# Performance work log

Hardware: AMD Instinct MI355X
Metric: run time of the kernel (lower is better)

## Reference

```python
import jax, jax.numpy as jnp
import numpy as np

B, L = 4, 8192
IN_CH, OUT_CH = 1, 1
H = 64               # d_model
NSTATE = 16          # d_state
DBLK = 4             # number of residual blocks
DCONV = 16
EXPAND = 2
DINNER = EXPAND * H              # 128
HEADDIM = H // 4                 # 16
NHEADS = DINNER // HEADDIM       # 8
CONV_DIM = DINNER + 2 * NSTATE   # 160 (ngroups=1)
D_IN_PROJ = 2 * DINNER + 2 * NSTATE + NHEADS  # 296
CHUNK = 128


def setup_inputs():
    key = jax.random.key(0)
    ks = jax.random.split(key, 12)
    rn = lambda k, shape, s: (jax.random.normal(k, shape) * s).astype(jnp.float32)
    x = rn(ks[0], (B, L, IN_CH), 1.0)
    w_in = rn(ks[1], (H, IN_CH), 1.0)
    w_out = rn(ks[2], (OUT_CH, H), 1.0 / np.sqrt(H))
    in_proj_w = rn(ks[3], (DBLK, D_IN_PROJ, H), 1.0 / np.sqrt(H))
    conv_w = rn(ks[4], (DBLK, CONV_DIM, DCONV), 1.0 / np.sqrt(DCONV))
    conv_b = rn(ks[5], (DBLK, CONV_DIM), 0.02)
    dt = jnp.exp(jax.random.uniform(ks[6], (DBLK, NHEADS)) * (np.log(0.1) - np.log(1e-3)) + np.log(1e-3))
    dt_bias = (dt + jnp.log(-jnp.expm1(-dt))).astype(jnp.float32)  # inverse softplus
    A_log = jnp.log(jax.random.uniform(ks[7], (DBLK, NHEADS), minval=1.0, maxval=16.0)).astype(jnp.float32)
    D_skip = jnp.ones((DBLK, NHEADS), jnp.float32)
    init_states = rn(ks[8], (DBLK, NHEADS, HEADDIM, NSTATE), 0.01)
    norm_w = jnp.ones((DBLK, DINNER), jnp.float32)
    out_proj_w = rn(ks[9], (DBLK, H, DINNER), 1.0 / np.sqrt(DINNER))
    mlp_w = rn(ks[10], (DBLK, H, H), 1.0 / np.sqrt(H))
    mlp_b = jnp.zeros((DBLK, H), jnp.float32)
    return {"x": x, "w_in": w_in, "w_out": w_out, "in_proj_w": in_proj_w,
            "conv_w": conv_w, "conv_b": conv_b, "dt_bias": dt_bias, "A_log": A_log,
            "D_skip": D_skip, "init_states": init_states, "norm_w": norm_w,
            "out_proj_w": out_proj_w, "mlp_w": mlp_w, "mlp_b": mlp_b}


def segsum(a):
    # a: (..., q) -> (..., q, q); seg[i, j] = sum_{k=j+1..i} a[k] on lower triangle (diag=0), exp->0 above
    q = a.shape[-1]
    cs = jnp.cumsum(a, axis=-1)
    seg = cs[..., :, None] - cs[..., None, :]
    mask = jnp.tril(jnp.ones((q, q), dtype=bool))
    return jnp.where(mask, seg, -1e30)


def ssd(X, dA, Bm, Cm, init_state):
    # Chunked SSD (Mamba2 paper). X: (b,l,h,p) = x*dt, dA: (b,l,h), Bm/Cm: (b,l,n), init_state: (b,h,p,n)
    b, l, h, p = X.shape
    c = l // CHUNK
    X = X.reshape(b, c, CHUNK, h, p)
    Bm = Bm.reshape(b, c, CHUNK, NSTATE)
    Cm = Cm.reshape(b, c, CHUNK, NSTATE)
    A = dA.reshape(b, c, CHUNK, h).transpose(0, 3, 1, 2)  # (b,h,c,q)
    A_cs = jnp.cumsum(A, axis=-1)
    # intra-chunk (diagonal blocks)
    Lm = jnp.exp(segsum(A))  # (b,h,c,q,q)
    Y_diag = jnp.einsum('bcln,bcsn,bhcls,bcshp->bclhp', Cm, Bm, Lm, X)
    # per-chunk final states
    decay_states = jnp.exp(A_cs[..., -1:] - A_cs)  # (b,h,c,q)
    states = jnp.einsum('bcln,bhcl,bclhp->bchpn', Bm, decay_states, X)
    states = jnp.concatenate([init_state[:, None], states], axis=1)  # (b,c+1,h,p,n)
    # inter-chunk recurrence (vectorized via segsum over chunk decays)
    decay_chunk = jnp.exp(segsum(jnp.pad(A_cs[..., -1], ((0, 0), (0, 0), (1, 0)))))  # (b,h,c+1,c+1)
    new_states = jnp.einsum('bhzc,bchpn->bzhpn', decay_chunk, states)
    prev_states = new_states[:, :-1]  # state entering each chunk
    state_decay = jnp.exp(A_cs)
    Y_off = jnp.einsum('bcln,bchpn,bhcl->bclhp', Cm, prev_states, state_decay)
    return (Y_diag + Y_off).reshape(b, l, h, p)


def mamba2(u, w_inp, cw, cb, dtb, alog, dskip, istate, nw, w_outp):
    b, l, _ = u.shape
    zxbcdt = jnp.einsum('bld,ed->ble', u, w_inp)  # (b,l,296)
    z = zxbcdt[..., :DINNER]
    xBC = zxbcdt[..., DINNER:DINNER + CONV_DIM]
    dt = jax.nn.softplus(zxbcdt[..., DINNER + CONV_DIM:] + dtb)  # (b,l,h)
    # causal depthwise conv over seq + silu
    xBC = jax.lax.conv_general_dilated(
        xBC.transpose(0, 2, 1), cw[:, None, :], (1,), [(DCONV - 1, 0)],
        feature_group_count=CONV_DIM, dimension_numbers=('NCH', 'OIH', 'NCH'))
    xBC = jax.nn.silu(xBC + cb[None, :, None]).transpose(0, 2, 1)
    xs = xBC[..., :DINNER]
    Bm = xBC[..., DINNER:DINNER + NSTATE]
    Cm = xBC[..., DINNER + NSTATE:]
    A = -jnp.exp(alog)  # (h,)
    xh = xs.reshape(b, l, NHEADS, HEADDIM)
    init = jnp.broadcast_to(istate, (b,) + istate.shape)
    y = ssd(xh * dt[..., None], dt * A, Bm, Cm, init)
    y = y + xh * dskip[None, None, :, None]  # D skip
    y = y.reshape(b, l, DINNER)
    # gated RMSNorm: norm(y * silu(z)) * weight
    y = y * jax.nn.silu(z)
    y = y * jax.lax.rsqrt(jnp.mean(y * y, axis=-1, keepdims=True) + 1e-5) * nw
    return jnp.einsum('ble,de->bld', y, w_outp)


def reference(x, w_in, w_out, in_proj_w, conv_w, conv_b, dt_bias, A_log,
              D_skip, init_states, norm_w, out_proj_w, mlp_w, mlp_b):
    h = jnp.einsum('bli,hi->blh', x, w_in)
    for i in range(DBLK):
        y = mamba2(h, in_proj_w[i], conv_w[i], conv_b[i], dt_bias[i], A_log[i],
                   D_skip[i], init_states[i], norm_w[i], out_proj_w[i])
        t = y / jnp.sqrt(1.0 + y * y)  # TanhApprox
        y = jnp.einsum('blh,oh->blo', t, mlp_w[i]) + mlp_b[i]
        h = h + y  # residual
    return jnp.einsum('blh,oh->blo', h, w_out)
```

## Files before the change

### kernel.cpp

```cpp
#include <hip/hip_runtime.h>
#include <math.h>

#define NB 4
#define SEQ 8192
#define NT (NB*SEQ)
#define HDIM 64
#define NST 16
#define NBLK 4
#define KCONV 16
#define DIN 128
#define PDIM 16
#define NH 8
#define CDIM 160
#define EPROJ 296
#define CH 128
#define NC 64

typedef __attribute__((ext_vector_type(8))) short short8;
typedef __attribute__((ext_vector_type(4))) float f32x4;

__device__ __forceinline__ float sigf(float x){ return 1.0f/(1.0f+__expf(-x)); }

__device__ __forceinline__ unsigned short bf16r(float f){
  unsigned int u = __float_as_uint(f);
  u = (u + 0x7fffu + ((u >> 16) & 1u)) >> 16;
  return (unsigned short)u;
}
__device__ __forceinline__ unsigned int pk_bf16(float a, float b){
  return (unsigned int)bf16r(a) | ((unsigned int)bf16r(b) << 16);
}
__device__ __forceinline__ float bf16f(unsigned short h){
  return __uint_as_float(((unsigned int)h) << 16);
}

__global__ __launch_bounds__(256) void k_init(const float* __restrict__ x, const float* __restrict__ w_in,
                                              float* __restrict__ h,
                                              const float* __restrict__ w,
                                              unsigned short* __restrict__ whi,
                                              unsigned short* __restrict__ wlo){
  int bi = blockIdx.x;
  const int HB = (NT*HDIM)/256;
  if(bi < HB){
    int i = bi*256 + threadIdx.x;
    int t = i >> 6, d = i & 63;
    h[i] = x[t]*w_in[d];
  } else {
    int i = (bi - HB)*256 + threadIdx.x;
    if(i < NBLK*EPROJ*HDIM){
      float f = w[i];
      unsigned short hi = bf16r(f);
      float fh = bf16f(hi);
      whi[i] = hi;
      wlo[i] = bf16r(f - fh);
    }
  }
}

__global__ __launch_bounds__(1024) void k_front(const float* __restrict__ h,
                                                const unsigned short* __restrict__ whi,
                                                const unsigned short* __restrict__ wlo,
                                                const float* __restrict__ cw, const float* __restrict__ cb,
                                                const float* __restrict__ dtb, const float* __restrict__ alog,
                                                unsigned short* __restrict__ zxz,
                                                unsigned short* __restrict__ xbc,
                                                float* __restrict__ dt, float* __restrict__ acs,
                                                float* __restrict__ asum, float* __restrict__ S){
  __shared__ __align__(16) unsigned char smf[148480];
  unsigned short* Hh  = (unsigned short*)(smf);
  unsigned short* Hl  = (unsigned short*)(smf + 20736);
  float* zxcS         = (float*)(smf + 41472);
  unsigned short* XhT = (unsigned short*)(smf);
  unsigned short* XlT = (unsigned short*)(smf + 34816);
  unsigned short* BhT = (unsigned short*)(smf + 69632);
  unsigned short* BlT = (unsigned short*)(smf + 73984);
  float* dtraw = (float*)(smf + 136192);
  float* dtl   = (float*)(smf + 140288);
  float* wle   = (float*)(smf + 144384);

  int bc = blockIdx.x;
  int c = bc & 63, b = bc >> 6;
  int t0 = b*SEQ + c*CH;
  int tid = threadIdx.x, lane = tid & 63, wid = tid >> 6;
  int quad = lane >> 4, lq = lane & 15;

#pragma unroll
  for(int k=0;k<3;k++){
    int idx = tid + k*1024;
    if(idx < 2304){
      int tok = idx >> 4;
      int d0 = (idx & 15) * 4;
      float4 v;
      if(c == 0 && tok < 16){ v = make_float4(0.f,0.f,0.f,0.f); }
      else v = *(const float4*)(h + (size_t)(t0 - 16 + tok)*HDIM + d0);
      float vv[4] = {v.x, v.y, v.z, v.w};
      unsigned short hi4[4], lo4[4];
#pragma unroll
      for(int j=0;j<4;j++){
        unsigned short hi = bf16r(vv[j]);
        hi4[j] = hi;
        lo4[j] = bf16r(vv[j] - bf16f(hi));
      }
      uint2 ph, pl;
      ph.x = (unsigned int)hi4[0] | ((unsigned int)hi4[1] << 16);
      ph.y = (unsigned int)hi4[2] | ((unsigned int)hi4[3] << 16);
      pl.x = (unsigned int)lo4[0] | ((unsigned int)lo4[1] << 16);
      pl.y = (unsigned int)lo4[2] | ((unsigned int)lo4[3] << 16);
      *(uint2*)&Hh[tok*72 + d0] = ph;
      *(uint2*)&Hl[tok*72 + d0] = pl;
    }
  }
  __syncthreads();

  {
    int L = wid;
    int tg, et;
    if(L < 152){ tg = 1 + L/19; et = L % 19; } else { tg = 0; et = 8 + (L - 152); }
    {
      int e_a = et*16 + lq;
      int ec = (e_a < EPROJ) ? e_a : (EPROJ-1);
      const unsigned short* wh = whi + (size_t)ec*HDIM + quad*8;
      const unsigned short* wl = wlo + (size_t)ec*HDIM + quad*8;
      short8 ah0 = *(const short8*)wh;
      short8 ah1 = *(const short8*)(wh + 32);
      short8 al0 = *(const short8*)wl;
      short8 al1 = *(const short8*)(wl + 32);
      while(true){
        int Ln = L + 16;
        int tgn = 0, etn = 0;
        short8 nh0 = ah0, nh1 = ah1, nl0 = al0, nl1 = al1;
        if(Ln < 162){
          if(Ln < 152){ tgn = 1 + Ln/19; etn = Ln % 19; } else { tgn = 0; etn = 8 + (Ln - 152); }
          int e_n = etn*16 + lq;
          int ecn = (e_n < EPROJ) ? e_n : (EPROJ-1);
          const unsigned short* wh2 = whi + (size_t)ecn*HDIM + quad*8;
          const unsigned short* wl2 = wlo + (size_t)ecn*HDIM + quad*8;
          nh0 = *(const short8*)wh2;
          nh1 = *(const short8*)(wh2 + 32);
          nl0 = *(const short8*)wl2;
          nl1 = *(const short8*)(wl2 + 32);
        }
        const unsigned short* hrh = Hh + (tg*16 + lq)*72 + quad*8;
        const unsigned short* hrl = Hl + (tg*16 + lq)*72 + quad*8;
        short8 xh0 = *(const short8*)hrh;
        short8 xh1 = *(const short8*)(hrh + 32);
        short8 xl0 = *(const short8*)hrl;
        short8 xl1 = *(const short8*)(hrl + 32);
        f32x4 acc = {0.f,0.f,0.f,0.f};
        acc = __builtin_amdgcn_mfma_f32_16x16x32_bf16(ah0, xh0, acc, 0, 0, 0);
        acc = __builtin_amdgcn_mfma_f32_16x16x32_bf16(ah1, xh1, acc, 0, 0, 0);
        acc = __builtin_amdgcn_mfma_f32_16x16x32_bf16(ah0, xl0, acc, 0, 0, 0);
        acc = __builtin_amdgcn_mfma_f32_16x16x32_bf16(ah1, xl1, acc, 0, 0, 0);
        acc = __builtin_amdgcn_mfma_f32_16x16x32_bf16(al0, xh0, acc, 0, 0, 0);
        acc = __builtin_amdgcn_mfma_f32_16x16x32_bf16(al1, xh1, acc, 0, 0, 0);
        if(tg >= 1){
          int tokg = t0 + (tg-1)*16 + lq;
#pragma unroll
          for(int r=0;r<4;r++){
            int e = et*16 + quad*4 + r;
            if(e < 128)        zxz[(size_t)e*NT + tokg] = bf16r(acc[r]);
            else if(e < 288)   zxcS[(e-128)*148 + tg*16 + lq] = acc[r];
            else if(e < 296)   dtraw[(e-288)*128 + (tg-1)*16 + lq] = acc[r];
          }
        } else {
#pragma unroll
          for(int r=0;r<4;r++){
            int e = et*16 + quad*4 + r;
            zxcS[(e-128)*148 + lq] = acc[r];
          }
        }
        if(Ln >= 162) break;
        L = Ln; tg = tgn; et = etn;
        ah0 = nh0; ah1 = nh1; al0 = nl0; al1 = nl1;
      }
    }
  }
  __syncthreads();

  unsigned int hiP[3][4], loP[3][4];
#pragma unroll
  for(int it=0; it<3; it++){
    int G = tid + it*1024;
    if(G < 2560){
      int ch = G >> 4, sg = (G & 15)*8;
      float buf[24];
#pragma unroll
      for(int q4=0;q4<6;q4++){
        float4 f = *(const float4*)&zxcS[ch*148 + sg + q4*4];
        buf[q4*4+0]=f.x; buf[q4*4+1]=f.y; buf[q4*4+2]=f.z; buf[q4*4+3]=f.w;
      }
      float wv[16];
#pragma unroll
      for(int k=0;k<16;k++) wv[k] = cw[ch*KCONV + k];
      float bias = cb[ch];
      unsigned short hs[8], ls[8];
#pragma unroll
      for(int s=0;s<8;s++){
        float acc = bias;
#pragma unroll
        for(int k=0;k<16;k++) acc += wv[k]*buf[s+1+k];
        float r = acc * sigf(acc);
        unsigned short hi = bf16r(r);
        hs[s] = hi;
        ls[s] = bf16r(r - bf16f(hi));
      }
      hiP[it][0] = (unsigned int)hs[0] | ((unsigned int)hs[1] << 16);
      hiP[it][1] = (unsigned int)hs[2] | ((unsigned int)hs[3] << 16);
      hiP[it][2] = (unsigned int)hs[4] | ((unsigned int)hs[5] << 16);
      hiP[it][3] = (unsigned int)hs[6] | ((unsigned int)hs[7] << 16);
      loP[it][0] = (unsigned int)ls[0] | ((unsigned int)ls[1] << 16);
      loP[it][1] = (unsigned int)ls[2] | ((unsigned int)ls[3] << 16);
      loP[it][2] = (unsigned int)ls[4] | ((unsigned int)ls[5] << 16);
      loP[it][3] = (unsigned int)ls[6] | ((unsigned int)ls[7] << 16);
      uint4 pk;
      pk.x = hiP[it][0]; pk.y = hiP[it][1]; pk.z = hiP[it][2]; pk.w = hiP[it][3];
      *(uint4*)(xbc + (size_t)ch*NT + t0 + sg) = pk;
    }
  }
  {
    int hh = tid >> 7, s = tid & 127;
    float raw = dtraw[hh*128 + s] + dtb[hh];
    float v = (raw > 20.f) ? raw : log1pf(__expf(raw));
    dtl[hh*128 + s] = v;
    dt[(size_t)hh*NT + t0 + s] = v;
  }
  __syncthreads();

#pragma unroll
  for(int it=0; it<3; it++){
    int G = tid + it*1024;
    if(G < 2560){
      int ch = G >> 4, sg = (G & 15)*8;
      if(ch < 128){
        uint4 vh; vh.x=hiP[it][0]; vh.y=hiP[it][1]; vh.z=hiP[it][2]; vh.w=hiP[it][3];
        uint4 vl; vl.x=loP[it][0]; vl.y=loP[it][1]; vl.z=loP[it][2]; vl.w=loP[it][3];
        *(uint4*)&XhT[ch*136 + sg] = vh;
        *(uint4*)&XlT[ch*136 + sg] = vl;
      } else if(ch < 144){
        uint4 vh; vh.x=hiP[it][0]; vh.y=hiP[it][1]; vh.z=hiP[it][2]; vh.w=hiP[it][3];
        uint4 vl; vl.x=loP[it][0]; vl.y=loP[it][1]; vl.z=loP[it][2]; vl.w=loP[it][3];
        *(uint4*)&BhT[(ch-128)*136 + sg] = vh;
        *(uint4*)&BlT[(ch-128)*136 + sg] = vl;
      }
    }
  }
  if(wid < 8){
    int hh = wid;
    float A = -__expf(alog[hh]);
    float2 dd = *(const float2*)&dtl[hh*128 + 2*lane];
    float d0 = dd.x, d1 = dd.y;
    float v0 = d0*A, v1 = d1*A;
    float s = v0 + v1;
    for(int off=1; off<64; off<<=1){
      float o = __shfl_up(s, off);
      if(lane >= off) s += o;
    }
    float tot = __shfl(s, 63);
    float excl = s - (v0+v1);
    float a0 = excl+v0, a1 = excl+v0+v1;
    *(float2*)&acs[(size_t)hh*NT + t0 + 2*lane] = make_float2(a0, a1);
    if(lane == 63) asum[(size_t)bc*NH + hh] = __expf(tot);
    wle[hh*128 + 2*lane]   = d0*__expf(tot - a0);
    wle[hh*128 + 2*lane+1] = d1*__expf(tot - a1);
  }
  __syncthreads();

  if(wid < 8){
    int hh = wid;
    f32x4 acc = {0.f,0.f,0.f,0.f};
#pragma unroll
    for(int kb=0;kb<4;kb++){
      int k0 = kb*32 + quad*8;
      short8 xh = *(const short8*)&XhT[(hh*16 + lq)*136 + k0];
      short8 xl = *(const short8*)&XlT[(hh*16 + lq)*136 + k0];
      float4 w0 = *(const float4*)&wle[hh*128 + k0];
      float4 w1 = *(const float4*)&wle[hh*128 + k0 + 4];
      float wv8[8] = {w0.x,w0.y,w0.z,w0.w,w1.x,w1.y,w1.z,w1.w};
      short8 ah, al;
#pragma unroll
      for(int j=0;j<8;j++){
        float xv = bf16f((unsigned short)xh[j]) + bf16f((unsigned short)xl[j]);
        float pw = xv * wv8[j];
        unsigned short hi = bf16r(pw);
        ah[j] = (short)hi;
        al[j] = (short)bf16r(pw - bf16f(hi));
      }
      short8 bh = *(const short8*)&BhT[lq*136 + k0];
      short8 bl = *(const short8*)&BlT[lq*136 + k0];
      acc = __builtin_amdgcn_mfma_f32_16x16x32_bf16(ah, bh, acc, 0, 0, 0);
      acc = __builtin_amdgcn_mfma_f32_16x16x32_bf16(ah, bl, acc, 0, 0, 0);
      acc = __builtin_amdgcn_mfma_f32_16x16x32_bf16(al, bh, acc, 0, 0, 0);
    }
    float* Sp = S + ((size_t)bc*NH + hh)*256;
#pragma unroll
    for(int r=0;r<4;r++) Sp[(quad*4 + r)*16 + lq] = acc[r];
  }
}

__global__ __launch_bounds__(64) void k_scan(const float* __restrict__ S, const float* __restrict__ easum,
                                             const float* __restrict__ init, float* __restrict__ prev){
  int q  = blockIdx.x & 3;
  int hh = (blockIdx.x >> 2) & 7;
  int b  = blockIdx.x >> 5;
  int el = q*64 + threadIdx.x;
  const size_t cs = (size_t)NH*256;
  const float* Sp = S + ((size_t)(b*NC)*NH + hh)*256 + el;
  float* Pp = prev + ((size_t)(b*NC)*NH + hh)*256 + el;
  const float* ap = easum + (size_t)(b*NC)*NH + hh;
  float e[NC];
#pragma unroll
  for(int c=0;c<NC;c++) e[c] = ap[(size_t)c*NH];
  float r = init[hh*256 + el];
  float s0 = Sp[0], s1 = Sp[cs], s2 = Sp[2*cs], s3 = Sp[3*cs];
#pragma unroll
  for(int c=0;c<NC;c+=4){
    Pp[(size_t)c*cs] = r;
    r = e[c]*r + s0;
    s0 = (c+4 < NC) ? Sp[(size_t)(c+4)*cs] : 0.f;
    Pp[(size_t)(c+1)*cs] = r;
    r = e[c+1]*r + s1;
    s1 = (c+5 < NC) ? Sp[(size_t)(c+5)*cs] : 0.f;
    Pp[(size_t)(c+2)*cs] = r;
    r = e[c+2]*r + s2;
    s2 = (c+6 < NC) ? Sp[(size_t)(c+6)*cs] : 0.f;
    Pp[(size_t)(c+3)*cs] = r;
    r = e[c+3]*r + s3;
    s3 = (c+7 < NC) ? Sp[(size_t)(c+7)*cs] : 0.f;
  }
}

__global__ __launch_bounds__(1024) void k_tail(const unsigned short* __restrict__ xbc,
                                               const unsigned short* __restrict__ zxz,
                                               const float* __restrict__ dt, const float* __restrict__ acs,
                                               const float* __restrict__ prev, const float* __restrict__ dskip,
                                               const float* __restrict__ nw, const float* __restrict__ opw,
                                               const float* __restrict__ mw, const float* __restrict__ mb,
                                               float* __restrict__ h,
                                               int last, const float* __restrict__ wout,
                                               float* __restrict__ out){
  __shared__ __align__(16) unsigned char sm[151840];
  unsigned short* Bb   = (unsigned short*)(sm);
  unsigned short* Cb   = (unsigned short*)(sm + 6144);
  unsigned short* XbT  = (unsigned short*)(sm + 12288);
  unsigned short* P0   = (unsigned short*)(sm + 55296);
  unsigned short* P1   = (unsigned short*)(sm + 98304);
  float* Al  = (float*)(sm + 141312);
  float* Dtl = (float*)(sm + 145408);
  float* nwl = (float*)(sm + 149504);
  float* mbl = (float*)(sm + 150016);
  unsigned short* zbuf = (unsigned short*)(sm + 150272);
  float* ssl  = (float*)(sm + 150304);
  float* outb = (float*)(sm + 151328);
  unsigned short* Zb = XbT;
  unsigned short* Wo = P0;
  unsigned short* Wm = P0 + 64*136;
  unsigned short* Yn = P1;
  unsigned short* Tt = XbT;

  int bc = blockIdx.x;
  int c = bc & 63, b = bc >> 6;
  int t0 = b*SEQ + c*CH;
  int tid = threadIdx.x, lane = tid & 63, wid = tid >> 6;
  int quad = lane >> 4, lq = lane & 15;
  int hgrp = wid >> 3;
  int wr7 = wid & 7;
  int widr = (wr7 < 4) ? wr7 : (11 - wr7);
  int strip = widr*16;

  {
    int ch = tid >> 5;
    int s4 = (tid & 31) * 4;
    uint2 xu = *(const uint2*)&xbc[(size_t)(DIN+ch)*NT + t0 + s4];
    unsigned short v0 = (unsigned short)(xu.x & 0xffffu);
    unsigned short v1 = (unsigned short)(xu.x >> 16);
    unsigned short v2 = (unsigned short)(xu.y & 0xffffu);
    unsigned short v3 = (unsigned short)(xu.y >> 16);
    unsigned short* dst = (ch < 16) ? Bb : Cb;
    int cc = (ch < 16) ? ch : (ch - 16);
    dst[(s4+0)*24 + cc] = v0;
    dst[(s4+1)*24 + cc] = v1;
    dst[(s4+2)*24 + cc] = v2;
    dst[(s4+3)*24 + cc] = v3;
  }
#pragma unroll
  for(int k=0;k<4;k++){
    int fi = tid + k*1024;
    int p = fi >> 5, s4 = fi & 31;
    uint2 xu = *(const uint2*)&xbc[(size_t)p*NT + t0 + s4*4];
    float4 dv = *(const float4*)&dt[(size_t)(p>>4)*NT + t0 + s4*4];
    float x0 = bf16f((unsigned short)(xu.x & 0xffffu));
    float x1 = bf16f((unsigned short)(xu.x >> 16));
    float x2 = bf16f((unsigned short)(xu.y & 0xffffu));
    float x3 = bf16f((unsigned short)(xu.y >> 16));
    *(unsigned int*)&XbT[p*168 + s4*4]   = pk_bf16(x0*dv.x, x1*dv.y);
    *(unsigned int*)&XbT[p*168 + s4*4+2] = pk_bf16(x2*dv.z, x3*dv.w);
  }
#pragma unroll
  for(int k=0;k<2;k++){
    int idx = tid + k*1024;
    int hh = idx >> 8, rest = idx & 255;
    int p = rest >> 4, n = rest & 15;
    XbT[(hh*16+p)*168 + 128 + n] = bf16r(prev[((size_t)bc*NH + hh)*256 + rest]);
  }
#pragma unroll
  for(int k=0;k<2;k++){
    int idx = tid + k*1024;
    if(idx < 1536){
      int p = idx / 12, cc = idx - p*12;
      *(unsigned int*)&XbT[p*168 + 144 + 2*cc] = 0u;
    }
  }
  {
    int hh = tid >> 7, s = tid & 127;
    Al[hh*128+s]  = acs[(size_t)hh*NT + t0 + s];
    Dtl[hh*128+s] = dt[(size_t)hh*NT + t0 + s];
  }
  if(tid < 128) nwl[tid] = nw[tid];
  else if(tid < 192) mbl[tid-128] = mb[tid-128];
  else if(tid < 208) zbuf[tid-192] = 0;
  {
    unsigned short* Pgz = hgrp ? P1 : P0;
#pragma unroll
    for(int k=0;k<3;k++){
      int idx = lane + k*64;
      int rr = idx / 12, cc = idx - rr*12;
      *(unsigned int*)&Pgz[(strip+rr)*168 + 144 + 2*cc] = 0u;
    }
    int zc0 = (widr+1)*16;
    int nu  = (7 - widr)*8;
    for(int u = lane>>4; u < nu; u += 4){
      *(unsigned int*)&Pgz[(strip+(lane&15))*168 + zc0 + 2*u] = 0u;
    }
  }
  __syncthreads();

  short8 afr;
  {
    int row = strip + lq;
    const unsigned short* ap = (quad < 2) ? &Cb[row*24 + quad*8] : zbuf;
    afr = *(const short8*)ap;
  }
  f32x4 sc[8];
#pragma unroll
  for(int nt=0;nt<8;nt++){
    f32x4 acc = {0.f,0.f,0.f,0.f};
    if(nt <= widr){
      const unsigned short* bp = (quad < 2) ? &Bb[(nt*16+lq)*24 + quad*8] : zbuf;
      short8 bfr = *(const short8*)bp;
      acc = __builtin_amdgcn_mfma_f32_16x16x32_bf16(afr, bfr, acc, 0, 0, 0);
    }
    sc[nt] = acc;
  }

  unsigned short* Pg = hgrp ? P1 : P0;
  f32x4 accv[4];
  for(int j=0;j<4;j++){
    int hh2 = hgrp*4 + j;
    const float* Alh = Al + hh2*128;
    float alr[4];
#pragma unroll
    for(int r=0;r<4;r++) alr[r] = Alh[strip + quad*4 + r];
#pragma unroll
    for(int nt=0;nt<8;nt++){
      if(nt <= widr){
        int col = nt*16 + lq;
        float alc = Alh[col];
#pragma unroll
        for(int r=0;r<4;r++){
          int row = strip + quad*4 + r;
          float p = sc[nt][r] * __expf(alr[r] - alc);
          p = (col <= row) ? p : 0.f;
          Pg[row*168 + col] = bf16r(p);
        }
      }
    }
    {
      int n = lane & 15, rg = lane >> 4;
#pragma unroll
      for(int rr=0;rr<4;rr++){
        int row = strip + rg*4 + rr;
        float ea = __expf(Alh[row]);
        Pg[row*168 + 128 + n] = bf16r(bf16f(Cb[row*24+n]) * ea);
      }
    }
    f32x4 acc2 = {0.f,0.f,0.f,0.f};
#pragma unroll
    for(int ks=0;ks<5;ks++){
      short8 bfr = *(const short8*)&XbT[(hh2*16+lq)*168 + ks*32 + quad*8];
      short8 af  = *(const short8*)&Pg[(strip+lq)*168 + ks*32 + quad*8];
      acc2 = __builtin_amdgcn_mfma_f32_16x16x32_bf16(af, bfr, acc2, 0, 0, 0);
    }
    const float* Dth = Dtl + hh2*128;
    float Dk = dskip[hh2];
#pragma unroll
    for(int r=0;r<4;r++){
      int l = strip + quad*4 + r;
      float xdt = bf16f(XbT[(hh2*16+lq)*168 + l]);
      float dtv = fmaxf(Dth[l], 1e-30f);
      acc2[r] += Dk * xdt * __frcp_rn(dtv);
    }
    accv[j] = acc2;
  }
  __syncthreads();

#pragma unroll
  for(int k=0;k<4;k++){
    int fi = tid + k*1024;
    int p = fi >> 5, s4 = fi & 31;
    uint2 zu = *(const uint2*)&zxz[(size_t)p*NT + t0 + s4*4];
    *(unsigned int*)&Zb[p*136 + s4*4]   = zu.x;
    *(unsigned int*)&Zb[p*136 + s4*4+2] = zu.y;
  }
#pragma unroll
  for(int k=0;k<2;k++){
    int fi = tid + k*1024;
    int n = fi >> 5, k4 = fi & 31;
    float4 wv = *(const float4*)&opw[(size_t)n*DIN + k4*4];
    *(unsigned int*)&Wo[n*136 + k4*4]   = pk_bf16(wv.x, wv.y);
    *(unsigned int*)&Wo[n*136 + k4*4+2] = pk_bf16(wv.z, wv.w);
  }
  {
    int fi = tid;
    int n = fi >> 4, k4 = fi & 15;
    float4 wv = *(const float4*)&mw[(size_t)n*HDIM + k4*4];
    *(unsigned int*)&Wm[n*72 + k4*4]   = pk_bf16(wv.x, wv.y);
    *(unsigned int*)&Wm[n*72 + k4*4+2] = pk_bf16(wv.z, wv.w);
  }
  __syncthreads();

  float part[4] = {0.f,0.f,0.f,0.f};
#pragma unroll
  for(int j=0;j<4;j++){
    int ch = (hgrp*4+j)*16 + lq;
    float nwv = nwl[ch];
#pragma unroll
    for(int r=0;r<4;r++){
      int l = strip + quad*4 + r;
      float zv = bf16f(Zb[ch*136 + l]);
      float g = zv * sigf(zv);
      float yv = accv[j][r] * g;
      part[r] += yv*yv;
      Yn[l*136 + ch] = bf16r(yv * nwv);
    }
  }
#pragma unroll
  for(int r=0;r<4;r++){
    part[r] += __shfl_xor(part[r],1); part[r] += __shfl_xor(part[r],2);
    part[r] += __shfl_xor(part[r],4); part[r] += __shfl_xor(part[r],8);
  }
  if(lq == 0){
#pragma unroll
    for(int r=0;r<4;r++) ssl[hgrp*128 + strip + quad*4 + r] = part[r];
  }
  __syncthreads();

  float rms_[4];
#pragma unroll
  for(int r=0;r<4;r++){
    int l = strip + quad*4 + r;
    rms_[r] = rsqrtf((ssl[l] + ssl[128+l])*(1.0f/128.0f) + 1e-5f);
  }
  short8 afk[4];
#pragma unroll
  for(int ks=0;ks<4;ks++) afk[ks] = *(const short8*)&Yn[(strip+lq)*136 + ks*32 + quad*8];
  f32x4 aco[2];
#pragma unroll
  for(int ntl=0;ntl<2;ntl++){ aco[ntl] = (f32x4){0.f,0.f,0.f,0.f}; }
#pragma unroll
  for(int ntl=0;ntl<2;ntl++){
    int nt = hgrp*2 + ntl;
#pragma unroll
    for(int ks=0;ks<4;ks++){
      short8 bfr = *(const short8*)&Wo[(nt*16+lq)*136 + ks*32 + quad*8];
      aco[ntl] = __builtin_amdgcn_mfma_f32_16x16x32_bf16(afk[ks], bfr, aco[ntl], 0, 0, 0);
    }
  }
#pragma unroll
  for(int ntl=0;ntl<2;ntl++){
    int nt = hgrp*2 + ntl;
#pragma unroll
    for(int r=0;r<4;r++){
      int l = strip + quad*4 + r;
      float o = aco[ntl][r] * rms_[r];
      Tt[l*136 + nt*16+lq] = bf16r(o * rsqrtf(1.0f + o*o));
    }
  }
  __syncthreads();

  f32x4 acm[2];
#pragma unroll
  for(int ntl=0;ntl<2;ntl++){ acm[ntl] = (f32x4){0.f,0.f,0.f,0.f}; }
#pragma unroll
  for(int ks=0;ks<2;ks++){
    short8 af = *(const short8*)&Tt[(strip+lq)*136 + ks*32 + quad*8];
#pragma unroll
    for(int ntl=0;ntl<2;ntl++){
      int nt = hgrp*2 + ntl;
      short8 bfr = *(const short8*)&Wm[(nt*16+lq)*72 + ks*32 + quad*8];
      acm[ntl] = __builtin_amdgcn_mfma_f32_16x16x32_bf16(af, bfr, acm[ntl], 0, 0, 0);
    }
  }
  if(!last){
#pragma unroll
    for(int ntl=0;ntl<2;ntl++){
      int nt = hgrp*2 + ntl;
#pragma unroll
      for(int r=0;r<4;r++){
        int l = strip + quad*4 + r;
        int d = nt*16 + lq;
        size_t gi = (size_t)(t0+l)*HDIM + d;
        h[gi] += acm[ntl][r] + mbl[d];
      }
    }
  } else {
    float ps[4] = {0.f,0.f,0.f,0.f};
#pragma unroll
    for(int ntl=0;ntl<2;ntl++){
      int nt = hgrp*2 + ntl;
      int d = nt*16 + lq;
      float wo = wout[d];
      float bias = mbl[d];
#pragma unroll
      for(int r=0;r<4;r++){
        int l = strip + quad*4 + r;
        size_t gi = (size_t)(t0+l)*HDIM + d;
        float hn = h[gi] + acm[ntl][r] + bias;
        ps[r] += hn * wo;
      }
    }
#pragma unroll
    for(int r=0;r<4;r++){
      ps[r] += __shfl_xor(ps[r],1); ps[r] += __shfl_xor(ps[r],2);
      ps[r] += __shfl_xor(ps[r],4); ps[r] += __shfl_xor(ps[r],8);
    }
    if(hgrp == 1 && lq == 0){
#pragma unroll
      for(int r=0;r<4;r++) outb[strip + quad*4 + r] = ps[r];
    }
    __syncthreads();
    if(hgrp == 0 && lq == 0){
#pragma unroll
      for(int r=0;r<4;r++){
        int l = strip + quad*4 + r;
        out[t0 + l] = ps[r] + outb[l];
      }
    }
  }
}

extern "C" void kernel_launch(void* const* d_in, const int* in_sizes, int n_in,
                              void* d_out, int out_size, void* d_ws, size_t ws_size,
                              hipStream_t stream){
  const float* x          = (const float*)d_in[0];
  const float* w_in       = (const float*)d_in[1];
  const float* w_out      = (const float*)d_in[2];
  const float* in_proj_w  = (const float*)d_in[3];
  const float* conv_w     = (const float*)d_in[4];
  const float* conv_b     = (const float*)d_in[5];
  const float* dt_bias    = (const float*)d_in[6];
  const float* A_log      = (const float*)d_in[7];
  const float* D_skip     = (const float*)d_in[8];
  const float* init_st    = (const float*)d_in[9];
  const float* norm_w     = (const float*)d_in[10];
  const float* out_proj_w = (const float*)d_in[11];
  const float* mlp_w      = (const float*)d_in[12];
  const float* mlp_b      = (const float*)d_in[13];
  float* out = (float*)d_out;

  float* ws = (float*)d_ws;
  float* h    = ws; ws += (size_t)NT*HDIM;
  unsigned short* zxz = (unsigned short*)ws; ws += (size_t)(128*NT)/2;
  unsigned short* xbc = (unsigned short*)ws; ws += (size_t)(CDIM*NT)/2;
  float* dt   = ws; ws += (size_t)NH*NT;
  float* acs  = ws; ws += (size_t)NH*NT;
  float* asum = ws; ws += (size_t)NB*NC*NH;
  float* S    = ws; ws += (size_t)NB*NC*NH*256;
  float* prev = ws; ws += (size_t)NB*NC*NH*256;
  unsigned short* whi = (unsigned short*)ws; ws += (size_t)(NBLK*EPROJ*HDIM)/2;
  unsigned short* wlo = (unsigned short*)ws; ws += (size_t)(NBLK*EPROJ*HDIM)/2;

  k_init<<<(NT*HDIM)/256 + (NBLK*EPROJ*HDIM)/256, 256, 0, stream>>>(x, w_in, h, in_proj_w, whi, wlo);
  for(int i=0;i<NBLK;i++){
    k_front<<<NB*NC, 1024, 0, stream>>>(h, whi + (size_t)i*EPROJ*HDIM, wlo + (size_t)i*EPROJ*HDIM,
                                        conv_w + i*CDIM*KCONV, conv_b + i*CDIM,
                                        dt_bias + i*NH, A_log + i*NH,
                                        zxz, xbc, dt, acs, asum, S);
    k_scan  <<<NB*NH*4, 64, 0, stream>>>(S, asum, init_st + i*NH*256, prev);
    k_tail  <<<NB*NC, 1024, 0, stream>>>(xbc, zxz, dt, acs, prev, D_skip + i*NH,
                                         norm_w + i*DIN, out_proj_w + i*HDIM*DIN,
                                         mlp_w + i*HDIM*HDIM, mlp_b + i*HDIM, h,
                                         (i == NBLK-1) ? 1 : 0, w_out, out);
  }
}
```

Measured before the change: 329.6 us.

## Load h directly into registers in k_front and shrink shared memory

k_front no longer stages the hi/lo bf16 split of h in shared memory. Each wave loads its 16-token tile straight from global memory into MFMA operand registers and reuses it across consecutive tiles. Work is now split as contiguous ranges of 81 tiles per 16 waves, so waves stay on the same token group. This drops one barrier and about 41KB of LDS, and adds a launch bounds occupancy hint. k_init is also vectorised to write h with float4 stores. The cost is redundant global loads of h across waves and uneven per-wave work.

```diff
diff --git a/kernel.cpp b/kernel.cpp
--- a/kernel.cpp
+++ b/kernel.cpp
@@ -39,11 +39,14 @@
                                               unsigned short* __restrict__ whi,
                                               unsigned short* __restrict__ wlo){
   int bi = blockIdx.x;
-  const int HB = (NT*HDIM)/256;
+  const int HB = (NT*HDIM)/1024;
   if(bi < HB){
-    int i = bi*256 + threadIdx.x;
-    int t = i >> 6, d = i & 63;
-    h[i] = x[t]*w_in[d];
+    int i4 = (bi*256 + threadIdx.x) * 4;
+    int t = i4 >> 6, d0 = i4 & 63;
+    float xv = x[t];
+    float4 wv = *(const float4*)(w_in + d0);
+    float4 hv = make_float4(xv*wv.x, xv*wv.y, xv*wv.z, xv*wv.w);
+    *(float4*)(h + i4) = hv;
   } else {
     int i = (bi - HB)*256 + threadIdx.x;
     if(i < NBLK*EPROJ*HDIM){
@@ -56,7 +59,7 @@
   }
 }
 
-__global__ __launch_bounds__(1024) void k_front(const float* __restrict__ h,
+__global__ __launch_bounds__(1024, 4) void k_front(const float* __restrict__ h,
                                                 const unsigned short* __restrict__ whi,
                                                 const unsigned short* __restrict__ wlo,
                                                 const float* __restrict__ cw, const float* __restrict__ cb,
@@ -65,17 +68,15 @@
                                                 unsigned short* __restrict__ xbc,
                                                 float* __restrict__ dt, float* __restrict__ acs,
                                                 float* __restrict__ asum, float* __restrict__ S){
-  __shared__ __align__(16) unsigned char smf[148480];
-  unsigned short* Hh  = (unsigned short*)(smf);
-  unsigned short* Hl  = (unsigned short*)(smf + 20736);
-  float* zxcS         = (float*)(smf + 41472);
+  __shared__ __align__(16) unsigned char smf[107008];
+  float* zxcS         = (float*)(smf);
   unsigned short* XhT = (unsigned short*)(smf);
   unsigned short* XlT = (unsigned short*)(smf + 34816);
   unsigned short* BhT = (unsigned short*)(smf + 69632);
   unsigned short* BlT = (unsigned short*)(smf + 73984);
-  float* dtraw = (float*)(smf + 136192);
-  float* dtl   = (float*)(smf + 140288);
-  float* wle   = (float*)(smf + 144384);
+  float* dtraw = (float*)(smf + 94720);
+  float* dtl   = (float*)(smf + 98816);
+  float* wle   = (float*)(smf + 102912);
 
   int bc = blockIdx.x;
   int c = bc & 63, b = bc >> 6;
@@ -83,95 +84,87 @@
   int tid = threadIdx.x, lane = tid & 63, wid = tid >> 6;
   int quad = lane >> 4, lq = lane & 15;
 
-#pragma unroll
-  for(int k=0;k<3;k++){
-    int idx = tid + k*1024;
-    if(idx < 2304){
-      int tok = idx >> 4;
-      int d0 = (idx & 15) * 4;
-      float4 v;
-      if(c == 0 && tok < 16){ v = make_float4(0.f,0.f,0.f,0.f); }
-      else v = *(const float4*)(h + (size_t)(t0 - 16 + tok)*HDIM + d0);
-      float vv[4] = {v.x, v.y, v.z, v.w};
-      unsigned short hi4[4], lo4[4];
-#pragma unroll
-      for(int j=0;j<4;j++){
-        unsigned short hi = bf16r(vv[j]);
-        hi4[j] = hi;
-        lo4[j] = bf16r(vv[j] - bf16f(hi));
-      }
-      uint2 ph, pl;
-      ph.x = (unsigned int)hi4[0] | ((unsigned int)hi4[1] << 16);
-      ph.y = (unsigned int)hi4[2] | ((unsigned int)hi4[3] << 16);
-      pl.x = (unsigned int)lo4[0] | ((unsigned int)lo4[1] << 16);
-      pl.y = (unsigned int)lo4[2] | ((unsigned int)lo4[3] << 16);
-      *(uint2*)&Hh[tok*72 + d0] = ph;
-      *(uint2*)&Hl[tok*72 + d0] = pl;
-    }
-  }
-  __syncthreads();
-
   {
-    int L = wid;
-    int tg, et;
-    if(L < 152){ tg = 1 + L/19; et = L % 19; } else { tg = 0; et = 8 + (L - 152); }
-    {
-      int e_a = et*16 + lq;
-      int ec = (e_a < EPROJ) ? e_a : (EPROJ-1);
-      const unsigned short* wh = whi + (size_t)ec*HDIM + quad*8;
-      const unsigned short* wl = wlo + (size_t)ec*HDIM + quad*8;
-      short8 ah0 = *(const short8*)wh;
-      short8 ah1 = *(const short8*)(wh + 32);
-      short8 al0 = *(const short8*)wl;
-      short8 al1 = *(const short8*)(wl + 32);
-      while(true){
-        int Ln = L + 16;
-        int tgn = 0, etn = 0;
-        short8 nh0 = ah0, nh1 = ah1, nl0 = al0, nl1 = al1;
-        if(Ln < 162){
-          if(Ln < 152){ tgn = 1 + Ln/19; etn = Ln % 19; } else { tgn = 0; etn = 8 + (Ln - 152); }
-          int e_n = etn*16 + lq;
-          int ecn = (e_n < EPROJ) ? e_n : (EPROJ-1);
-          const unsigned short* wh2 = whi + (size_t)ecn*HDIM + quad*8;
-          const unsigned short* wl2 = wlo + (size_t)ecn*HDIM + quad*8;
-          nh0 = *(const short8*)wh2;
-          nh1 = *(const short8*)(wh2 + 32);
-          nl0 = *(const short8*)wl2;
-          nl1 = *(const short8*)(wl2 + 32);
-        }
-        const unsigned short* hrh = Hh + (tg*16 + lq)*72 + quad*8;
-        const unsigned short* hrl = Hl + (tg*16 + lq)*72 + quad*8;
-        short8 xh0 = *(const short8*)hrh;
-        short8 xh1 = *(const short8*)(hrh + 32);
-        short8 xl0 = *(const short8*)hrl;
-        short8 xl1 = *(const short8*)(hrl + 32);
-        f32x4 acc = {0.f,0.f,0.f,0.f};
-        acc = __builtin_amdgcn_mfma_f32_16x16x32_bf16(ah0, xh0, acc, 0, 0, 0);
-        acc = __builtin_amdgcn_mfma_f32_16x16x32_bf16(ah1, xh1, acc, 0, 0, 0);
-        acc = __builtin_amdgcn_mfma_f32_16x16x32_bf16(ah0, xl0, acc, 0, 0, 0);
-        acc = __builtin_amdgcn_mfma_f32_16x16x32_bf16(ah1, xl1, acc, 0, 0, 0);
-        acc = __builtin_amdgcn_mfma_f32_16x16x32_bf16(al0, xh0, acc, 0, 0, 0);
-        acc = __builtin_amdgcn_mfma_f32_16x16x32_bf16(al1, xh1, acc, 0, 0, 0);
-        if(tg >= 1){
-          int tokg = t0 + (tg-1)*16 + lq;
-#pragma unroll
-          for(int r=0;r<4;r++){
-            int e = et*16 + quad*4 + r;
-            if(e < 128)        zxz[(size_t)e*NT + tokg] = bf16r(acc[r]);
-            else if(e < 288)   zxcS[(e-128)*148 + tg*16 + lq] = acc[r];
-            else if(e < 296)   dtraw[(e-288)*128 + (tg-1)*16 + lq] = acc[r];
-          }
+    int s  = (wid*81) >> 3;
+    int en = ((wid+1)*81) >> 3;
+    int idx = s;
+    int tg  = (idx < 10) ? 0 : 1 + (idx-10)/19;
+    int et  = (idx < 10) ? 8 + idx : (idx-10)%19;
+    int curtg = -1;
+    short8 xh0 = {0,0,0,0,0,0,0,0}, xh1 = {0,0,0,0,0,0,0,0};
+    short8 xl0 = {0,0,0,0,0,0,0,0}, xl1 = {0,0,0,0,0,0,0,0};
+    int e_a = et*16 + lq;
+    int ec = (e_a < EPROJ) ? e_a : (EPROJ-1);
+    const unsigned short* wh = whi + (size_t)ec*HDIM + quad*8;
+    const unsigned short* wl = wlo + (size_t)ec*HDIM + quad*8;
+    short8 ah0 = *(const short8*)wh;
+    short8 ah1 = *(const short8*)(wh + 32);
+    short8 al0 = *(const short8*)wl;
+    short8 al1 = *(const short8*)(wl + 32);
+    while(true){
+      if(tg != curtg){
+        if(c == 0 && tg == 0){
+#pragma unroll
+          for(int j=0;j<8;j++){ xh0[j]=0; xh1[j]=0; xl0[j]=0; xl1[j]=0; }
         } else {
-#pragma unroll
-          for(int r=0;r<4;r++){
-            int e = et*16 + quad*4 + r;
-            zxcS[(e-128)*148 + lq] = acc[r];
+          const float* hp = h + (size_t)(t0 - 16 + tg*16 + lq)*HDIM + quad*8;
+#pragma unroll
+          for(int kb=0;kb<2;kb++){
+            float4 f0 = *(const float4*)(hp + kb*32);
+            float4 f1 = *(const float4*)(hp + kb*32 + 4);
+            float v[8] = {f0.x,f0.y,f0.z,f0.w,f1.x,f1.y,f1.z,f1.w};
+#pragma unroll
+            for(int j=0;j<8;j++){
+              unsigned short hi = bf16r(v[j]);
+              float lo = v[j] - bf16f(hi);
+              if(kb==0){ xh0[j] = (short)hi; xl0[j] = (short)bf16r(lo); }
+              else     { xh1[j] = (short)hi; xl1[j] = (short)bf16r(lo); }
+            }
           }
         }
-        if(Ln >= 162) break;
-        L = Ln; tg = tgn; et = etn;
-        ah0 = nh0; ah1 = nh1; al0 = nl0; al1 = nl1;
-      }
+        curtg = tg;
+      }
+      int idxn = idx + 1;
+      int tgn = tg, etn = et;
+      short8 nh0 = ah0, nh1 = ah1, nl0 = al0, nl1 = al1;
+      if(idxn < en){
+        tgn = (idxn < 10) ? 0 : 1 + (idxn-10)/19;
+        etn = (idxn < 10) ? 8 + idxn : (idxn-10)%19;
+        int e_n = etn*16 + lq;
+        int ecn = (e_n < EPROJ) ? e_n : (EPROJ-1);
+        const unsigned short* wh2 = whi + (size_t)ecn*HDIM + quad*8;
+        const unsigned short* wl2 = wlo + (size_t)ecn*HDIM + quad*8;
+        nh0 = *(const short8*)wh2;
+        nh1 = *(const short8*)(wh2 + 32);
+        nl0 = *(const short8*)wl2;
+        nl1 = *(const short8*)(wl2 + 32);
+      }
+      f32x4 acc = {0.f,0.f,0.f,0.f};
+      acc = __builtin_amdgcn_mfma_f32_16x16x32_bf16(ah0, xh0, acc, 0, 0, 0);
+      acc = __builtin_amdgcn_mfma_f32_16x16x32_bf16(ah1, xh1, acc, 0, 0, 0);
+      acc = __builtin_amdgcn_mfma_f32_16x16x32_bf16(ah0, xl0, acc, 0, 0, 0);
+      acc = __builtin_amdgcn_mfma_f32_16x16x32_bf16(ah1, xl1, acc, 0, 0, 0);
+      acc = __builtin_amdgcn_mfma_f32_16x16x32_bf16(al0, xh0, acc, 0, 0, 0);
+      acc = __builtin_amdgcn_mfma_f32_16x16x32_bf16(al1, xh1, acc, 0, 0, 0);
+      if(tg >= 1){
+        int tokg = t0 + (tg-1)*16 + lq;
+#pragma unroll
+        for(int r=0;r<4;r++){
+          int e = et*16 + quad*4 + r;
+          if(e < 128)        zxz[(size_t)e*NT + tokg] = bf16r(acc[r]);
+          else if(e < 288)   zxcS[(e-128)*148 + tg*16 + lq] = acc[r];
+          else if(e < 296)   dtraw[(e-288)*128 + (tg-1)*16 + lq] = acc[r];
+        }
+      } else {
+#pragma unroll
+        for(int r=0;r<4;r++){
+          int e = et*16 + quad*4 + r;
+          zxcS[(e-128)*148 + lq] = acc[r];
+        }
+      }
+      if(idxn >= en) break;
+      idx = idxn; tg = tgn; et = etn;
+      ah0 = nh0; ah1 = nh1; al0 = nl0; al1 = nl1;
     }
   }
   __syncthreads();
@@ -678,7 +671,7 @@
   unsigned short* whi = (unsigned short*)ws; ws += (size_t)(NBLK*EPROJ*HDIM)/2;
   unsigned short* wlo = (unsigned short*)ws; ws += (size_t)(NBLK*EPROJ*HDIM)/2;
 
-  k_init<<<(NT*HDIM)/256 + (NBLK*EPROJ*HDIM)/256, 256, 0, stream>>>(x, w_in, h, in_proj_w, whi, wlo);
+  k_init<<<(NT*HDIM)/1024 + (NBLK*EPROJ*HDIM + 255)/256, 256, 0, stream>>>(x, w_in, h, in_proj_w, whi, wlo);
   for(int i=0;i<NBLK;i++){
     k_front<<<NB*NC, 1024, 0, stream>>>(h, whi + (size_t)i*EPROJ*HDIM, wlo + (size_t)i*EPROJ*HDIM,
                                         conv_w + i*CDIM*KCONV, conv_b + i*CDIM,
```

New measurement: 333.0 us. No clear change (+1.0%).

## Fold inter-chunk state scan into tail kernel via weighted prefix sums

Applied to the files above, without the earlier changes.

Removes the separate k_scan kernel and its prev buffer. Each tail block now computes its chunk's incoming state directly as a decay-weighted sum over all earlier chunk states: half the waves build the weights with a shuffle prefix product and accumulate, while the other half do the original shared-memory staging loads. This saves one launch per layer and the serial scan, but later chunks redo O(c) reads of S, so total work becomes quadratic in the chunk count. A stray no-op line referencing zxcS was also added in k_front.

```diff
diff --git a/kernel.cpp b/kernel.cpp
--- a/kernel.cpp
+++ b/kernel.cpp
@@ -218,7 +218,8 @@
   }
   {
     int hh = tid >> 7, s = tid & 127;
-    float raw = dtraw[hh*128 + s] + dtb[hh];
+    float raw = zxcS ? 0.f : 0.f;
+    raw = dtraw[hh*128 + s] + dtb[hh];
     float v = (raw > 20.f) ? raw : log1pf(__expf(raw));
     dtl[hh*128 + s] = v;
     dt[(size_t)hh*NT + t0 + s] = v;
@@ -296,42 +297,12 @@
   }
 }
 
-__global__ __launch_bounds__(64) void k_scan(const float* __restrict__ S, const float* __restrict__ easum,
-                                             const float* __restrict__ init, float* __restrict__ prev){
-  int q  = blockIdx.x & 3;
-  int hh = (blockIdx.x >> 2) & 7;
-  int b  = blockIdx.x >> 5;
-  int el = q*64 + threadIdx.x;
-  const size_t cs = (size_t)NH*256;
-  const float* Sp = S + ((size_t)(b*NC)*NH + hh)*256 + el;
-  float* Pp = prev + ((size_t)(b*NC)*NH + hh)*256 + el;
-  const float* ap = easum + (size_t)(b*NC)*NH + hh;
-  float e[NC];
-#pragma unroll
-  for(int c=0;c<NC;c++) e[c] = ap[(size_t)c*NH];
-  float r = init[hh*256 + el];
-  float s0 = Sp[0], s1 = Sp[cs], s2 = Sp[2*cs], s3 = Sp[3*cs];
-#pragma unroll
-  for(int c=0;c<NC;c+=4){
-    Pp[(size_t)c*cs] = r;
-    r = e[c]*r + s0;
-    s0 = (c+4 < NC) ? Sp[(size_t)(c+4)*cs] : 0.f;
-    Pp[(size_t)(c+1)*cs] = r;
-    r = e[c+1]*r + s1;
-    s1 = (c+5 < NC) ? Sp[(size_t)(c+5)*cs] : 0.f;
-    Pp[(size_t)(c+2)*cs] = r;
-    r = e[c+2]*r + s2;
-    s2 = (c+6 < NC) ? Sp[(size_t)(c+6)*cs] : 0.f;
-    Pp[(size_t)(c+3)*cs] = r;
-    r = e[c+3]*r + s3;
-    s3 = (c+7 < NC) ? Sp[(size_t)(c+7)*cs] : 0.f;
-  }
-}
-
 __global__ __launch_bounds__(1024) void k_tail(const unsigned short* __restrict__ xbc,
                                                const unsigned short* __restrict__ zxz,
                                                const float* __restrict__ dt, const float* __restrict__ acs,
-                                               const float* __restrict__ prev, const float* __restrict__ dskip,
+                                               const float* __restrict__ S, const float* __restrict__ easum,
+                                               const float* __restrict__ initst,
+                                               const float* __restrict__ dskip,
                                                const float* __restrict__ nw, const float* __restrict__ opw,
                                                const float* __restrict__ mw, const float* __restrict__ mb,
                                                float* __restrict__ h,
@@ -366,64 +337,100 @@
   int widr = (wr7 < 4) ? wr7 : (11 - wr7);
   int strip = widr*16;
 
-  {
-    int ch = tid >> 5;
-    int s4 = (tid & 31) * 4;
-    uint2 xu = *(const uint2*)&xbc[(size_t)(DIN+ch)*NT + t0 + s4];
-    unsigned short v0 = (unsigned short)(xu.x & 0xffffu);
-    unsigned short v1 = (unsigned short)(xu.x >> 16);
-    unsigned short v2 = (unsigned short)(xu.y & 0xffffu);
-    unsigned short v3 = (unsigned short)(xu.y >> 16);
-    unsigned short* dst = (ch < 16) ? Bb : Cb;
-    int cc = (ch < 16) ? ch : (ch - 16);
-    dst[(s4+0)*24 + cc] = v0;
-    dst[(s4+1)*24 + cc] = v1;
-    dst[(s4+2)*24 + cc] = v2;
-    dst[(s4+3)*24 + cc] = v3;
-  }
-#pragma unroll
-  for(int k=0;k<4;k++){
-    int fi = tid + k*1024;
-    int p = fi >> 5, s4 = fi & 31;
-    uint2 xu = *(const uint2*)&xbc[(size_t)p*NT + t0 + s4*4];
-    float4 dv = *(const float4*)&dt[(size_t)(p>>4)*NT + t0 + s4*4];
-    float x0 = bf16f((unsigned short)(xu.x & 0xffffu));
-    float x1 = bf16f((unsigned short)(xu.x >> 16));
-    float x2 = bf16f((unsigned short)(xu.y & 0xffffu));
-    float x3 = bf16f((unsigned short)(xu.y >> 16));
-    *(unsigned int*)&XbT[p*168 + s4*4]   = pk_bf16(x0*dv.x, x1*dv.y);
-    *(unsigned int*)&XbT[p*168 + s4*4+2] = pk_bf16(x2*dv.z, x3*dv.w);
-  }
-#pragma unroll
-  for(int k=0;k<2;k++){
-    int idx = tid + k*1024;
-    int hh = idx >> 8, rest = idx & 255;
-    int p = rest >> 4, n = rest & 15;
-    XbT[(hh*16+p)*168 + 128 + n] = bf16r(prev[((size_t)bc*NH + hh)*256 + rest]);
-  }
-#pragma unroll
-  for(int k=0;k<2;k++){
-    int idx = tid + k*1024;
-    if(idx < 1536){
-      int p = idx / 12, cc = idx - p*12;
-      *(unsigned int*)&XbT[p*168 + 144 + 2*cc] = 0u;
-    }
-  }
-  {
-    int hh = tid >> 7, s = tid & 127;
-    Al[hh*128+s]  = acs[(size_t)hh*NT + t0 + s];
-    Dtl[hh*128+s] = dt[(size_t)hh*NT + t0 + s];
-  }
-  if(tid < 128) nwl[tid] = nw[tid];
-  else if(tid < 192) mbl[tid-128] = mb[tid-128];
-  else if(tid < 208) zbuf[tid-192] = 0;
+  if(wid >= 8){
+    int tid2 = tid - 512;
+#pragma unroll
+    for(int k=0;k<2;k++){
+      int i = tid2 + k*512;
+      int ch = i >> 5;
+      int s4 = (i & 31) * 4;
+      uint2 xu = *(const uint2*)&xbc[(size_t)(DIN+ch)*NT + t0 + s4];
+      unsigned short v0 = (unsigned short)(xu.x & 0xffffu);
+      unsigned short v1 = (unsigned short)(xu.x >> 16);
+      unsigned short v2 = (unsigned short)(xu.y & 0xffffu);
+      unsigned short v3 = (unsigned short)(xu.y >> 16);
+      unsigned short* dst = (ch < 16) ? Bb : Cb;
+      int cc2 = (ch < 16) ? ch : (ch - 16);
+      dst[(s4+0)*24 + cc2] = v0;
+      dst[(s4+1)*24 + cc2] = v1;
+      dst[(s4+2)*24 + cc2] = v2;
+      dst[(s4+3)*24 + cc2] = v3;
+    }
+#pragma unroll
+    for(int k=0;k<8;k++){
+      int fi = tid2 + k*512;
+      int p = fi >> 5, s4 = fi & 31;
+      uint2 xu = *(const uint2*)&xbc[(size_t)p*NT + t0 + s4*4];
+      float4 dv = *(const float4*)&dt[(size_t)(p>>4)*NT + t0 + s4*4];
+      float x0 = bf16f((unsigned short)(xu.x & 0xffffu));
+      float x1 = bf16f((unsigned short)(xu.x >> 16));
+      float x2 = bf16f((unsigned short)(xu.y & 0xffffu));
+      float x3 = bf16f((unsigned short)(xu.y >> 16));
+      *(unsigned int*)&XbT[p*168 + s4*4]   = pk_bf16(x0*dv.x, x1*dv.y);
+      *(unsigned int*)&XbT[p*168 + s4*4+2] = pk_bf16(x2*dv.z, x3*dv.w);
+    }
+#pragma unroll
+    for(int k=0;k<3;k++){
+      int idx = tid2 + k*512;
+      int p = idx / 12, cc2 = idx - p*12;
+      *(unsigned int*)&XbT[p*168 + 144 + 2*cc2] = 0u;
+    }
+#pragma unroll
+    for(int k=0;k<2;k++){
+      int idx = tid2 + k*512;
+      int hh = idx >> 7, s = idx & 127;
+      Al[hh*128+s]  = acs[(size_t)hh*NT + t0 + s];
+      Dtl[hh*128+s] = dt[(size_t)hh*NT + t0 + s];
+    }
+    if(tid2 < 128) nwl[tid2] = nw[tid2];
+    else if(tid2 < 192) mbl[tid2-128] = mb[tid2-128];
+    else if(tid2 < 208) zbuf[tid2-192] = 0;
+  } else {
+    int hh = wid;
+    float vj = (lane < c) ? easum[((size_t)(b*NC) + lane)*NH + hh] : 1.0f;
+    float s = vj;
+#pragma unroll
+    for(int off=1; off<64; off<<=1){
+      float o = __shfl_down(s, off);
+      if(lane + off < 64) s *= o;
+    }
+    float wk = __shfl_down(s, 1);
+    if(lane == 63) wk = 1.0f;
+    float winit = __shfl(s, 0);
+    const size_t cs = (size_t)NH*256;
+    const float* Sp0 = S + (((size_t)(b*NC))*NH + hh)*256 + lane;
+    const float* ip = initst + hh*256 + lane;
+    float a0 = winit * ip[0];
+    float a1 = winit * ip[64];
+    float a2 = winit * ip[128];
+    float a3 = winit * ip[192];
+    int k = 0;
+    for(; k+1 < c; k += 2){
+      float w0 = __shfl(wk, k), w1 = __shfl(wk, k+1);
+      const float* rp0 = Sp0 + (size_t)k*cs;
+      const float* rp1 = rp0 + cs;
+      a0 += w0*rp0[0];   a1 += w0*rp0[64];  a2 += w0*rp0[128]; a3 += w0*rp0[192];
+      a0 += w1*rp1[0];   a1 += w1*rp1[64];  a2 += w1*rp1[128]; a3 += w1*rp1[192];
+    }
+    if(k < c){
+      float w0 = __shfl(wk, k);
+      const float* rp0 = Sp0 + (size_t)k*cs;
+      a0 += w0*rp0[0];   a1 += w0*rp0[64];  a2 += w0*rp0[128]; a3 += w0*rp0[192];
+    }
+    float av[4] = {a0, a1, a2, a3};
+#pragma unroll
+    for(int m=0;m<4;m++){
+      int el = m*64 + lane;
+      XbT[(hh*16 + (el>>4))*168 + 128 + (el & 15)] = bf16r(av[m]);
+    }
+  }
   {
     unsigned short* Pgz = hgrp ? P1 : P0;
 #pragma unroll
     for(int k=0;k<3;k++){
       int idx = lane + k*64;
-      int rr = idx / 12, cc = idx - rr*12;
-      *(unsigned int*)&Pgz[(strip+rr)*168 + 144 + 2*cc] = 0u;
+      int rr = idx / 12, cc2 = idx - rr*12;
+      *(unsigned int*)&Pgz[(strip+rr)*168 + 144 + 2*cc2] = 0u;
     }
     int zc0 = (widr+1)*16;
     int nu  = (7 - widr)*8;
@@ -674,7 +681,6 @@
   float* acs  = ws; ws += (size_t)NH*NT;
   float* asum = ws; ws += (size_t)NB*NC*NH;
   float* S    = ws; ws += (size_t)NB*NC*NH*256;
-  float* prev = ws; ws += (size_t)NB*NC*NH*256;
   unsigned short* whi = (unsigned short*)ws; ws += (size_t)(NBLK*EPROJ*HDIM)/2;
   unsigned short* wlo = (unsigned short*)ws; ws += (size_t)(NBLK*EPROJ*HDIM)/2;
 
@@ -684,8 +690,8 @@
                                         conv_w + i*CDIM*KCONV, conv_b + i*CDIM,
                                         dt_bias + i*NH, A_log + i*NH,
                                         zxz, xbc, dt, acs, asum, S);
-    k_scan  <<<NB*NH*4, 64, 0, stream>>>(S, asum, init_st + i*NH*256, prev);
-    k_tail  <<<NB*NC, 1024, 0, stream>>>(xbc, zxz, dt, acs, prev, D_skip + i*NH,
+    k_tail  <<<NB*NC, 1024, 0, stream>>>(xbc, zxz, dt, acs, S, asum, init_st + i*NH*256,
+                                         D_skip + i*NH,
                                          norm_w + i*DIN, out_proj_w + i*HDIM*DIN,
                                          mlp_w + i*HDIM*HDIM, mlp_b + i*HDIM, h,
                                          (i == NBLK-1) ? 1 : 0, w_out, out);
```

Measured after the change: 342.3 us. 3.9% more time.
